# Kernel optimization log

Measured on AMD Instinct MI355X. Metric: run time of the kernel, lower is better.

Reference implementation:

```python
import jax, jax.numpy as jnp
import numpy as np

N, E, DIN, DOUT = 50000, 625000, 128, 128


def setup_inputs() -> dict:
    key = jax.random.key(0)
    k = jax.random.split(key, 4)
    x = jax.random.normal(k[0], (N, DIN), dtype=jnp.float32)
    edge_index = jax.random.randint(k[1], (2, E), 0, N, dtype=jnp.int32)
    s = 1.0 / np.sqrt(DIN)  # Glorot-ish init like torch Linear
    W_fwd = jax.random.uniform(k[2], (DIN, DOUT), jnp.float32, -s, s)
    W_bwd = jax.random.uniform(k[3], (DIN, DOUT), jnp.float32, -s, s)
    b_fwd = jnp.zeros((DOUT,), jnp.float32)
    b_bwd = jnp.zeros((DOUT,), jnp.float32)
    return {"x": x, "edge_index": edge_index, "W_fwd": W_fwd, "b_fwd": b_fwd,
            "W_bwd": W_bwd, "b_bwd": b_bwd}


def gcn_conv(x, W, b, src, dst, n):
    """PyG GCNConv: add self-loops, symmetric degree norm, gather-scatter aggregate."""
    loops = jnp.arange(n, dtype=src.dtype)
    src2 = jnp.concatenate([src, loops])  # [E+N]
    dst2 = jnp.concatenate([dst, loops])
    ones = jnp.ones(src2.shape[0], dtype=x.dtype)
    deg = jax.ops.segment_sum(ones, dst2, num_segments=n)  # in-degree incl. self-loop
    dinv = jnp.where(deg > 0, jax.lax.rsqrt(deg), 0.0)
    norm = dinv[src2] * dinv[dst2]  # [E+N]
    h = x @ W  # [N, DOUT] dense GEMM before message passing
    msgs = h[src2] * norm[:, None]  # gather + scale, [E+N, DOUT]
    out = jax.ops.segment_sum(msgs, dst2, num_segments=n)  # scatter-add
    return out + b


def reference(x, edge_index, W_fwd, b_fwd, W_bwd, b_bwd):
    src, dst = edge_index[0], edge_index[1]
    n = x.shape[0]
    x_forward = gcn_conv(x, W_fwd, b_fwd, src, dst, n)
    # reversed edge direction for the backward diffusion conv
    x_backward = gcn_conv(x, W_bwd, b_bwd, dst, src, n)
    # dropout omitted (eval mode / deterministic reference)
    return jax.nn.relu(x_forward + x_backward)
```

## Files before the change

### kernel.cpp

```cpp
#include <hip/hip_runtime.h>
#include <hip/hip_bf16.h>
#include <cstdint>

static constexpr int BLK      = 256;
static constexpr int CAP      = 40;
static constexpr int BINSHIFT = 8;
static constexpr int BINNODES = 1 << BINSHIFT;
static constexpr int BINCAP   = BINNODES * CAP / 2;
static constexpr int EPB      = 2048;
static constexpr int OVMAX    = 1024;
static constexpr int NB2MAX   = 512;

typedef __attribute__((ext_vector_type(8))) short bf16x8;
typedef __attribute__((ext_vector_type(4))) float f32x4;

__device__ __forceinline__ float bf16lo(uint32_t u) { return __uint_as_float(u << 16); }
__device__ __forceinline__ float bf16hi(uint32_t u) { return __uint_as_float(u & 0xffff0000u); }
__device__ __forceinline__ unsigned short f2bf(float f) {
    __hip_bfloat16 h = __float2bfloat16(f);
    return *(unsigned short*)&h;
}

__global__ __launch_bounds__(BLK) void k_bin(
        const int* __restrict__ src, const int* __restrict__ dst, int ne,
        uint32_t* __restrict__ pair, int* __restrict__ gcnt,
        int* __restrict__ ovcnt, int* __restrict__ ovlist, int nbins) {
    __shared__ uint32_t stage[EPB * 2];
    __shared__ int hist[NB2MAX];
    __shared__ int lofs[NB2MAX];
    __shared__ int gbase[NB2MAX];
    __shared__ int chunk[NB2MAX / 8];
    const int tid = threadIdx.x, bid = blockIdx.x;
    const int nb2 = 2 * nbins;
    for (int i = tid; i < nb2; i += BLK) hist[i] = 0;
    __syncthreads();

    int s[8], d[8];
    const int e0 = bid * EPB + tid;
#pragma unroll
    for (int k = 0; k < 8; ++k) {
        int e = e0 + k * BLK;
        bool v = e < ne;
        s[k] = v ? src[e] : -1;
        d[k] = v ? dst[e] : -1;
        if (v) {
            atomicAdd(&hist[d[k] >> BINSHIFT], 1);
            atomicAdd(&hist[nbins + (s[k] >> BINSHIFT)], 1);
        }
    }
    __syncthreads();

    const int nch = (nb2 + 7) >> 3;
    if (tid < nch) {
        int a = 0, base = tid << 3;
#pragma unroll
        for (int k = 0; k < 8; ++k) { int idx = base + k; if (idx < nb2) a += hist[idx]; }
        chunk[tid] = a;
    }
    __syncthreads();
    if (tid == 0) { int a = 0; for (int c = 0; c < nch; ++c) { int t = chunk[c]; chunk[c] = a; a += t; } }
    __syncthreads();
    for (int i = tid; i < nb2; i += BLK) {
        int a = chunk[i >> 3];
        for (int k = (i >> 3) << 3; k < i; ++k) a += hist[k];
        lofs[i] = a;
    }
    __syncthreads();
    for (int i = tid; i < nb2; i += BLK) {
        int c = hist[i];
        gbase[i] = c ? atomicAdd(&gcnt[i], c) : 0;
        hist[i] = lofs[i];
    }
    __syncthreads();
#pragma unroll
    for (int k = 0; k < 8; ++k) {
        if (s[k] >= 0) {
            int b0 = d[k] >> BINSHIFT;
            int p0 = atomicAdd(&hist[b0], 1);
            stage[p0] = ((uint32_t)d[k] << 16) | (uint32_t)s[k];
            int b1 = nbins + (s[k] >> BINSHIFT);
            int p1 = atomicAdd(&hist[b1], 1);
            stage[p1] = ((uint32_t)s[k] << 16) | (uint32_t)d[k];
        }
    }
    __syncthreads();
    int nval = ne - bid * EPB; if (nval > EPB) nval = EPB; if (nval < 0) nval = 0;
    const int total = 2 * nval;
    for (int i = tid; i < total; i += BLK) {
        int lo = 0, hi = nb2 - 1;
        while (lo < hi) { int mid = (lo + hi + 1) >> 1; if (lofs[mid] <= i) lo = mid; else hi = mid - 1; }
        int gidx = gbase[lo] + (i - lofs[lo]);
        if (gidx < BINCAP)
            pair[(size_t)lo * BINCAP + gidx] = stage[i];
        else {
            int node = (int)(stage[i] >> 16);
            int q = atomicAdd(ovcnt, 1);
            if (q < OVMAX) ovlist[q] = (node << 1) | (lo >= nbins ? 1 : 0);
        }
    }
}

__global__ __launch_bounds__(BLK) void k_build_conv(
        uint32_t* __restrict__ pair, const int* __restrict__ gcnt,
        int* __restrict__ cnt_f, int* __restrict__ cnt_b,
        float* __restrict__ dinv_f, float* __restrict__ dinv_b,
        int* __restrict__ ovcnt, int* __restrict__ ovlist,
        const float* __restrict__ x, uint32_t* __restrict__ xb32, int nxw, int gxc,
        const float* __restrict__ Wf, const float* __restrict__ Wb,
        unsigned short* __restrict__ WTf, unsigned short* __restrict__ WTb,
        int n, int nbins) {
    const int bid = blockIdx.x, tid = threadIdx.x;
    const int nb2 = 2 * nbins;
    if (bid < nb2) {
        __shared__ unsigned short buck[BINNODES * CAP];
        __shared__ int lcnt[BINNODES];
        lcnt[tid] = 0;
        __syncthreads();
        int count = gcnt[bid]; if (count > BINCAP) count = BINCAP;
        const uint32_t* pb = pair + (size_t)bid * BINCAP;
        const int dir = bid >= nbins ? 1 : 0;
        for (int i = tid; i < count; i += BLK) {
            uint32_t p = pb[i];
            int l = (p >> 16) & (BINNODES - 1);
            int r = atomicAdd(&lcnt[l], 1);
            if (r < CAP) buck[l * CAP + r] = (unsigned short)(p & 0xffffu);
            else {
                int q = atomicAdd(ovcnt, 1);
                if (q < OVMAX)
                    ovlist[q] = (((((bid - dir * nbins) << BINSHIFT) + l)) << 1) | dir;
            }
        }
        __syncthreads();
        const int node = ((bid - dir * nbins) << BINSHIFT) + tid;
        if (node < n) {
            int c = lcnt[tid];
            if (dir) { cnt_b[node] = c; dinv_b[node] = rsqrtf(1.0f + (float)c); }
            else     { cnt_f[node] = c; dinv_f[node] = rsqrtf(1.0f + (float)c); }
        }
        uint32_t* seg = pair + (size_t)bid * BINCAP;
        const uint32_t* b32 = (const uint32_t*)buck;
        for (int i = tid; i < BINCAP; i += BLK) seg[i] = b32[i];
        return;
    }
    if (bid < nb2 + gxc) {
        int base = (bid - nb2) * 2048;
        int end = base + 2048; if (end > nxw) end = nxw;
        for (int i = base + tid; i < end; i += BLK) {
            float2 v = ((const float2*)x)[i];
            xb32[i] = ((uint32_t)f2bf(v.y) << 16) | (uint32_t)f2bf(v.x);
        }
        return;
    }
    int wb = bid - nb2 - gxc;
    for (int idx = wb * 2048 + tid; idx < (wb + 1) * 2048; idx += BLK) {
        int c = idx >> 7, k = idx & 127;
        WTf[c * 128 + k] = f2bf(Wf[k * 128 + c]);
        WTb[c * 128 + k] = f2bf(Wb[k * 128 + c]);
    }
}

__device__ __forceinline__ void accum_range(
        int j0, int j1, int ofs, float sc,
        const uint32_t* __restrict__ xb, int lane, float& a0, float& a1) {
    int j = j0;
    for (; j + 8 <= j1; j += 8) {
        int   o0 = __shfl(ofs, j + 0), o1 = __shfl(ofs, j + 1);
        int   o2 = __shfl(ofs, j + 2), o3 = __shfl(ofs, j + 3);
        int   o4 = __shfl(ofs, j + 4), o5 = __shfl(ofs, j + 5);
        int   o6 = __shfl(ofs, j + 6), o7 = __shfl(ofs, j + 7);
        float s0 = __shfl(sc, j + 0), s1 = __shfl(sc, j + 1);
        float s2 = __shfl(sc, j + 2), s3 = __shfl(sc, j + 3);
        float s4 = __shfl(sc, j + 4), s5 = __shfl(sc, j + 5);
        float s6 = __shfl(sc, j + 6), s7 = __shfl(sc, j + 7);
        uint32_t u0 = xb[(size_t)(o0 + lane)], u1 = xb[(size_t)(o1 + lane)];
        uint32_t u2 = xb[(size_t)(o2 + lane)], u3 = xb[(size_t)(o3 + lane)];
        uint32_t u4 = xb[(size_t)(o4 + lane)], u5 = xb[(size_t)(o5 + lane)];
        uint32_t u6 = xb[(size_t)(o6 + lane)], u7 = xb[(size_t)(o7 + lane)];
        a0 = fmaf(s0, bf16lo(u0), a0); a1 = fmaf(s0, bf16hi(u0), a1);
        a0 = fmaf(s1, bf16lo(u1), a0); a1 = fmaf(s1, bf16hi(u1), a1);
        a0 = fmaf(s2, bf16lo(u2), a0); a1 = fmaf(s2, bf16hi(u2), a1);
        a0 = fmaf(s3, bf16lo(u3), a0); a1 = fmaf(s3, bf16hi(u3), a1);
        a0 = fmaf(s4, bf16lo(u4), a0); a1 = fmaf(s4, bf16hi(u4), a1);
        a0 = fmaf(s5, bf16lo(u5), a0); a1 = fmaf(s5, bf16hi(u5), a1);
        a0 = fmaf(s6, bf16lo(u6), a0); a1 = fmaf(s6, bf16hi(u6), a1);
        a0 = fmaf(s7, bf16lo(u7), a0); a1 = fmaf(s7, bf16hi(u7), a1);
    }
    for (; j + 4 <= j1; j += 4) {
        int   o0 = __shfl(ofs, j + 0), o1 = __shfl(ofs, j + 1);
        int   o2 = __shfl(ofs, j + 2), o3 = __shfl(ofs, j + 3);
        float s0 = __shfl(sc, j + 0), s1 = __shfl(sc, j + 1);
        float s2 = __shfl(sc, j + 2), s3 = __shfl(sc, j + 3);
        uint32_t u0 = xb[(size_t)(o0 + lane)], u1 = xb[(size_t)(o1 + lane)];
        uint32_t u2 = xb[(size_t)(o2 + lane)], u3 = xb[(size_t)(o3 + lane)];
        a0 = fmaf(s0, bf16lo(u0), a0); a1 = fmaf(s0, bf16hi(u0), a1);
        a0 = fmaf(s1, bf16lo(u1), a0); a1 = fmaf(s1, bf16hi(u1), a1);
        a0 = fmaf(s2, bf16lo(u2), a0); a1 = fmaf(s2, bf16hi(u2), a1);
        a0 = fmaf(s3, bf16lo(u3), a0); a1 = fmaf(s3, bf16hi(u3), a1);
    }
    for (; j < j1; ++j) {
        int oj = __shfl(ofs, j); float sj = __shfl(sc, j);
        uint32_t uj = xb[(size_t)(oj + lane)];
        a0 = fmaf(sj, bf16lo(uj), a0); a1 = fmaf(sj, bf16hi(uj), a1);
    }
}

__global__ __launch_bounds__(BLK) void k_gather_agg(
        const int* __restrict__ cnt_f, const int* __restrict__ cnt_b,
        const unsigned short* __restrict__ adj_f,
        const unsigned short* __restrict__ adj_b,
        const float* __restrict__ dinv_f, const float* __restrict__ dinv_b,
        const uint32_t* __restrict__ xb32,
        uint32_t* __restrict__ agg32,
        int n, int gnode,
        const int* __restrict__ ovcnt, const int* __restrict__ ovlist,
        const int* __restrict__ src, const int* __restrict__ dst, int ne) {
    const int bid = blockIdx.x;
    if (bid < gnode) {
        const int wave = threadIdx.x >> 6;
        const int lane = threadIdx.x & 63;
        const int node = bid * 4 + wave;
        if (node >= n) return;

        int cf = cnt_f[node], cb = cnt_b[node];
        if (cf > CAP || cb > CAP) return;

        float dvsf = dinv_f[node], dvsb = dinv_b[node];
        uint32_t uv = xb32[(size_t)node * 64 + lane];
        float accf0 = dvsf * dvsf * bf16lo(uv), accf1 = dvsf * dvsf * bf16hi(uv);
        float accb0 = dvsb * dvsb * bf16lo(uv), accb1 = dvsb * dvsb * bf16hi(uv);

        const int mt = cf + cb;
        if (mt <= 64) {
            int ofs = 0; float sc = 0.f;
            if (lane < cf) {
                int nb = adj_f[node * CAP + lane];
                ofs = nb * 64;
                sc  = dvsf * dinv_f[nb];
            } else if (lane < mt) {
                int nb = adj_b[node * CAP + (lane - cf)];
                ofs = nb * 64;
                sc  = dvsb * dinv_b[nb];
            }
            accum_range(0,  cf, ofs, sc, xb32, lane, accf0, accf1);
            accum_range(cf, mt, ofs, sc, xb32, lane, accb0, accb1);
        } else {
            for (int j = 0; j < cf; ++j) {
                int nb = adj_f[node * CAP + j];
                float dj = dvsf * dinv_f[nb];
                uint32_t u = xb32[(size_t)nb * 64 + lane];
                accf0 = fmaf(dj, bf16lo(u), accf0); accf1 = fmaf(dj, bf16hi(u), accf1);
            }
            for (int j = 0; j < cb; ++j) {
                int nb = adj_b[node * CAP + j];
                float dj = dvsb * dinv_b[nb];
                uint32_t u = xb32[(size_t)nb * 64 + lane];
                accb0 = fmaf(dj, bf16lo(u), accb0); accb1 = fmaf(dj, bf16hi(u), accb1);
            }
        }
        agg32[(size_t)node * 128 + lane] =
            ((uint32_t)f2bf(accf1) << 16) | (uint32_t)f2bf(accf0);
        agg32[(size_t)node * 128 + 64 + lane] =
            ((uint32_t)f2bf(accb1) << 16) | (uint32_t)f2bf(accb0);
        return;
    }

    int nov = *ovcnt; if (nov > OVMAX) nov = OVMAX;
    if (nov == 0) return;
    __shared__ int lst[4096];
    __shared__ int lc;
    const int tid = threadIdx.x;
    for (int i = bid - gnode; i < nov; i += 8) {
        int node = ovlist[i] >> 1;
        for (int d2 = 0; d2 < 2; ++d2) {
            const int* key = d2 ? src : dst;
            const int* val = d2 ? dst : src;
            const float* dinv = d2 ? dinv_b : dinv_f;
            float dvs = dinv[node];
            float s0 = 0.f, s1 = 0.f;
            if (tid < 64) {
                uint32_t u = xb32[(size_t)node * 64 + tid];
                s0 = dvs * bf16lo(u); s1 = dvs * bf16hi(u);
            }
            for (int start = 0; start < ne; start += 4096) {
                if (tid == 0) lc = 0;
                __syncthreads();
                int end = min(start + 4096, ne);
                for (int e2 = start + tid; e2 < end; e2 += BLK)
                    if (key[e2] == node) { int q = atomicAdd(&lc, 1); lst[q] = val[e2]; }
                __syncthreads();
                int mm = lc;
                if (tid < 64) {
                    for (int j = 0; j < mm; ++j) {
                        int nb = lst[j];
                        float dv = dinv[nb];
                        uint32_t u = xb32[(size_t)nb * 64 + tid];
                        s0 = fmaf(dv, bf16lo(u), s0);
                        s1 = fmaf(dv, bf16hi(u), s1);
                    }
                }
                __syncthreads();
            }
            if (tid < 64) {
                float a0 = dvs * s0, a1 = dvs * s1;
                agg32[(size_t)node * 128 + d2 * 64 + tid] =
                    ((uint32_t)f2bf(a1) << 16) | (uint32_t)f2bf(a0);
            }
            __syncthreads();
        }
    }
}

__global__ __launch_bounds__(BLK) void k_gemm_out(
        const unsigned short* __restrict__ agg,
        const unsigned short* __restrict__ WTf,
        const unsigned short* __restrict__ WTb,
        const float* __restrict__ bfv, const float* __restrict__ bbv,
        float* __restrict__ out, int n) {
    const int wave = threadIdx.x >> 6, lane = threadIdx.x & 63;
    const int wm = wave >> 1, wh = wave & 1;
    const int q = lane >> 4, t16 = lane & 15;
    const int m0 = blockIdx.x * 32 + wm * 16;
    int arow = m0 + t16; if (arow >= n) arow = n - 1;
    const unsigned short* ra = agg + (size_t)arow * 256;
    bf16x8 af[4], ab[4];
#pragma unroll
    for (int s = 0; s < 4; ++s) {
        af[s] = *(const bf16x8*)(ra + s * 32 + q * 8);
        ab[s] = *(const bf16x8*)(ra + 128 + s * 32 + q * 8);
    }
    __syncthreads();
#pragma unroll
    for (int t = 0; t < 4; ++t) {
        const int col = wh * 64 + t * 16 + t16;
        const unsigned short* wrf = WTf + (size_t)col * 128;
        const unsigned short* wrb = WTb + (size_t)col * 128;
        f32x4 c = {0.f, 0.f, 0.f, 0.f};
#pragma unroll
        for (int s = 0; s < 4; ++s)
            c = __builtin_amdgcn_mfma_f32_16x16x32_bf16(
                    af[s], *(const bf16x8*)(wrf + s * 32 + q * 8), c, 0, 0, 0);
#pragma unroll
        for (int s = 0; s < 4; ++s)
            c = __builtin_amdgcn_mfma_f32_16x16x32_bf16(
                    ab[s], *(const bf16x8*)(wrb + s * 32 + q * 8), c, 0, 0, 0);
        const float bias = bfv[col] + bbv[col];
#pragma unroll
        for (int r = 0; r < 4; ++r) {
            int row = m0 + q * 4 + r;
            if (row < n)
                out[(size_t)row * 128 + col] = fmaxf(c[r] + bias, 0.f);
        }
    }
}

extern "C" void kernel_launch(void* const* d_in, const int* in_sizes, int n_in,
                              void* d_out, int out_size, void* d_ws, size_t ws_size,
                              hipStream_t stream) {
    const float* x  = (const float*)d_in[0];
    const int*   ei = (const int*)d_in[1];
    const float* Wf = (const float*)d_in[2];
    const float* bf = (const float*)d_in[3];
    const float* Wb = (const float*)d_in[4];
    const float* bb = (const float*)d_in[5];

    const int n  = in_sizes[0] / 128;
    const int ne = in_sizes[1] / 2;
    const int* src = ei;
    const int* dst = ei + ne;
    float* out = (float*)d_out;

    const int nbins = (n + BINNODES - 1) >> BINSHIFT;
    const int nb2   = 2 * nbins;

    char* w = (char*)d_ws;
    uint32_t* pair = (uint32_t*)w;              w += (size_t)nb2 * BINCAP * 4;
    uint32_t* xb32 = (uint32_t*)w;              w += (size_t)n * 64 * 4;
    float* dinv_f = (float*)w;                  w += (size_t)n * 4;
    float* dinv_b = (float*)w;                  w += (size_t)n * 4;
    unsigned short* WTf = (unsigned short*)w;   w += 128 * 128 * 2;
    unsigned short* WTb = (unsigned short*)w;   w += 128 * 128 * 2;
    int* cnt_f = (int*)w;                       w += (size_t)n * 4;
    int* cnt_b = (int*)w;                       w += (size_t)n * 4;
    int* gcnt = (int*)w;                        w += (size_t)nb2 * 4;
    int* ovcnt = (int*)w;                       w += 8 * 4;
    int* ovlist = (int*)w;                      w += OVMAX * 4;

    const unsigned short* adj_f = (const unsigned short*)pair;
    const unsigned short* adj_b = adj_f + (size_t)nbins * BINNODES * CAP;
    uint32_t* agg32 = (uint32_t*)d_out;

    const int gbin  = (ne + EPB - 1) / EPB;
    const int gxc   = (n * 64 + 2047) / 2048;
    const int gnode = (n + 3) / 4;
    const int ggo   = (n + 31) / 32;

    hipMemsetAsync(gcnt, 0, (size_t)(nb2 + 8) * 4, stream);

    k_bin<<<gbin, BLK, 0, stream>>>(src, dst, ne, pair, gcnt, ovcnt, ovlist, nbins);

    k_build_conv<<<nb2 + gxc + 8, BLK, 0, stream>>>(pair, gcnt,
                                                    cnt_f, cnt_b, dinv_f, dinv_b,
                                                    ovcnt, ovlist,
                                                    x, xb32, n * 64, gxc,
                                                    Wf, Wb, WTf, WTb, n, nbins);

    k_gather_agg<<<gnode + 8, BLK, 0, stream>>>(cnt_f, cnt_b, adj_f, adj_b,
                                                dinv_f, dinv_b, xb32,
                                                agg32, n, gnode,
                                                ovcnt, ovlist, src, dst, ne);

    k_gemm_out<<<ggo, BLK, 0, stream>>>((const unsigned short*)agg32,
                                        WTf, WTb, bf, bb, out, n);
}
```

Baseline: 199.4 us.

## Fuse x/W conversion into binning kernel and pack per-node metadata

Moves the bf16 conversion of x and the W transposes from the build kernel into the binning kernel, so that independent work overlaps with edge binning and the build kernel only handles the bins. In binning, a per-item bin index is kept in shared memory in place of a binary search over the offsets. Per-node count and dinv for both directions are packed into one 16-byte meta record read with a single load, and the gather step preloads neighbor indices and dinv before the degree check, with forward and backward edges fixed to wave halves of 32 lanes. The trade is more shared memory in the binning kernel, a zero-fill of the bucket array, and a fast path now limited to 32 edges per direction.

```diff
diff --git a/kernel.cpp b/kernel.cpp
--- a/kernel.cpp
+++ b/kernel.cpp
@@ -16,134 +16,99 @@
 
 __device__ __forceinline__ float bf16lo(uint32_t u) { return __uint_as_float(u << 16); }
 __device__ __forceinline__ float bf16hi(uint32_t u) { return __uint_as_float(u & 0xffff0000u); }
+__device__ __forceinline__ float bf16f(unsigned short u) { return __uint_as_float((uint32_t)u << 16); }
 __device__ __forceinline__ unsigned short f2bf(float f) {
     __hip_bfloat16 h = __float2bfloat16(f);
     return *(unsigned short*)&h;
 }
 
-__global__ __launch_bounds__(BLK) void k_bin(
+__global__ __launch_bounds__(BLK) void k_bin_conv(
         const int* __restrict__ src, const int* __restrict__ dst, int ne,
         uint32_t* __restrict__ pair, int* __restrict__ gcnt,
-        int* __restrict__ ovcnt, int* __restrict__ ovlist, int nbins) {
-    __shared__ uint32_t stage[EPB * 2];
-    __shared__ int hist[NB2MAX];
-    __shared__ int lofs[NB2MAX];
-    __shared__ int gbase[NB2MAX];
-    __shared__ int chunk[NB2MAX / 8];
-    const int tid = threadIdx.x, bid = blockIdx.x;
-    const int nb2 = 2 * nbins;
-    for (int i = tid; i < nb2; i += BLK) hist[i] = 0;
-    __syncthreads();
-
-    int s[8], d[8];
-    const int e0 = bid * EPB + tid;
-#pragma unroll
-    for (int k = 0; k < 8; ++k) {
-        int e = e0 + k * BLK;
-        bool v = e < ne;
-        s[k] = v ? src[e] : -1;
-        d[k] = v ? dst[e] : -1;
-        if (v) {
-            atomicAdd(&hist[d[k] >> BINSHIFT], 1);
-            atomicAdd(&hist[nbins + (s[k] >> BINSHIFT)], 1);
-        }
-    }
-    __syncthreads();
-
-    const int nch = (nb2 + 7) >> 3;
-    if (tid < nch) {
-        int a = 0, base = tid << 3;
-#pragma unroll
-        for (int k = 0; k < 8; ++k) { int idx = base + k; if (idx < nb2) a += hist[idx]; }
-        chunk[tid] = a;
-    }
-    __syncthreads();
-    if (tid == 0) { int a = 0; for (int c = 0; c < nch; ++c) { int t = chunk[c]; chunk[c] = a; a += t; } }
-    __syncthreads();
-    for (int i = tid; i < nb2; i += BLK) {
-        int a = chunk[i >> 3];
-        for (int k = (i >> 3) << 3; k < i; ++k) a += hist[k];
-        lofs[i] = a;
-    }
-    __syncthreads();
-    for (int i = tid; i < nb2; i += BLK) {
-        int c = hist[i];
-        gbase[i] = c ? atomicAdd(&gcnt[i], c) : 0;
-        hist[i] = lofs[i];
-    }
-    __syncthreads();
-#pragma unroll
-    for (int k = 0; k < 8; ++k) {
-        if (s[k] >= 0) {
-            int b0 = d[k] >> BINSHIFT;
-            int p0 = atomicAdd(&hist[b0], 1);
-            stage[p0] = ((uint32_t)d[k] << 16) | (uint32_t)s[k];
-            int b1 = nbins + (s[k] >> BINSHIFT);
-            int p1 = atomicAdd(&hist[b1], 1);
-            stage[p1] = ((uint32_t)s[k] << 16) | (uint32_t)d[k];
-        }
-    }
-    __syncthreads();
-    int nval = ne - bid * EPB; if (nval > EPB) nval = EPB; if (nval < 0) nval = 0;
-    const int total = 2 * nval;
-    for (int i = tid; i < total; i += BLK) {
-        int lo = 0, hi = nb2 - 1;
-        while (lo < hi) { int mid = (lo + hi + 1) >> 1; if (lofs[mid] <= i) lo = mid; else hi = mid - 1; }
-        int gidx = gbase[lo] + (i - lofs[lo]);
-        if (gidx < BINCAP)
-            pair[(size_t)lo * BINCAP + gidx] = stage[i];
-        else {
-            int node = (int)(stage[i] >> 16);
-            int q = atomicAdd(ovcnt, 1);
-            if (q < OVMAX) ovlist[q] = (node << 1) | (lo >= nbins ? 1 : 0);
-        }
-    }
-}
-
-__global__ __launch_bounds__(BLK) void k_build_conv(
-        uint32_t* __restrict__ pair, const int* __restrict__ gcnt,
-        int* __restrict__ cnt_f, int* __restrict__ cnt_b,
-        float* __restrict__ dinv_f, float* __restrict__ dinv_b,
-        int* __restrict__ ovcnt, int* __restrict__ ovlist,
+        int* __restrict__ ovcnt, int* __restrict__ ovlist, int nbins, int gbin,
         const float* __restrict__ x, uint32_t* __restrict__ xb32, int nxw, int gxc,
         const float* __restrict__ Wf, const float* __restrict__ Wb,
-        unsigned short* __restrict__ WTf, unsigned short* __restrict__ WTb,
-        int n, int nbins) {
+        unsigned short* __restrict__ WTf, unsigned short* __restrict__ WTb) {
     const int bid = blockIdx.x, tid = threadIdx.x;
-    const int nb2 = 2 * nbins;
-    if (bid < nb2) {
-        __shared__ unsigned short buck[BINNODES * CAP];
-        __shared__ int lcnt[BINNODES];
-        lcnt[tid] = 0;
-        __syncthreads();
-        int count = gcnt[bid]; if (count > BINCAP) count = BINCAP;
-        const uint32_t* pb = pair + (size_t)bid * BINCAP;
-        const int dir = bid >= nbins ? 1 : 0;
-        for (int i = tid; i < count; i += BLK) {
-            uint32_t p = pb[i];
-            int l = (p >> 16) & (BINNODES - 1);
-            int r = atomicAdd(&lcnt[l], 1);
-            if (r < CAP) buck[l * CAP + r] = (unsigned short)(p & 0xffffu);
+    if (bid < gbin) {
+        __shared__ uint32_t stage[EPB * 2];
+        __shared__ unsigned short binof[EPB * 2];
+        __shared__ int hist[NB2MAX];
+        __shared__ int lofs[NB2MAX];
+        __shared__ int gbase[NB2MAX];
+        __shared__ int chunk[NB2MAX / 8];
+        const int nb2 = 2 * nbins;
+        for (int i = tid; i < nb2; i += BLK) hist[i] = 0;
+        __syncthreads();
+
+        int s[8], d[8];
+        const int e0 = bid * EPB + tid;
+#pragma unroll
+        for (int k = 0; k < 8; ++k) {
+            int e = e0 + k * BLK;
+            bool v = e < ne;
+            s[k] = v ? src[e] : -1;
+            d[k] = v ? dst[e] : -1;
+            if (v) {
+                atomicAdd(&hist[d[k] >> BINSHIFT], 1);
+                atomicAdd(&hist[nbins + (s[k] >> BINSHIFT)], 1);
+            }
+        }
+        __syncthreads();
+
+        const int nch = (nb2 + 7) >> 3;
+        if (tid < nch) {
+            int a = 0, base = tid << 3;
+#pragma unroll
+            for (int k = 0; k < 8; ++k) { int idx = base + k; if (idx < nb2) a += hist[idx]; }
+            chunk[tid] = a;
+        }
+        __syncthreads();
+        if (tid == 0) { int a = 0; for (int c = 0; c < nch; ++c) { int t = chunk[c]; chunk[c] = a; a += t; } }
+        __syncthreads();
+        for (int i = tid; i < nb2; i += BLK) {
+            int a = chunk[i >> 3];
+            for (int k = (i >> 3) << 3; k < i; ++k) a += hist[k];
+            lofs[i] = a;
+        }
+        __syncthreads();
+        for (int i = tid; i < nb2; i += BLK) {
+            int c = hist[i];
+            gbase[i] = c ? atomicAdd(&gcnt[i], c) : 0;
+            hist[i] = lofs[i];
+        }
+        __syncthreads();
+#pragma unroll
+        for (int k = 0; k < 8; ++k) {
+            if (s[k] >= 0) {
+                int b0 = d[k] >> BINSHIFT;
+                int p0 = atomicAdd(&hist[b0], 1);
+                stage[p0] = ((uint32_t)d[k] << 16) | (uint32_t)s[k];
+                binof[p0] = (unsigned short)b0;
+                int b1 = nbins + (s[k] >> BINSHIFT);
+                int p1 = atomicAdd(&hist[b1], 1);
+                stage[p1] = ((uint32_t)s[k] << 16) | (uint32_t)d[k];
+                binof[p1] = (unsigned short)b1;
+            }
+        }
+        __syncthreads();
+        int nval = ne - bid * EPB; if (nval > EPB) nval = EPB; if (nval < 0) nval = 0;
+        const int total = 2 * nval;
+        for (int i = tid; i < total; i += BLK) {
+            int b = binof[i];
+            int gidx = gbase[b] + (i - lofs[b]);
+            if (gidx < BINCAP)
+                pair[(size_t)b * BINCAP + gidx] = stage[i];
             else {
+                int node = (int)(stage[i] >> 16);
                 int q = atomicAdd(ovcnt, 1);
-                if (q < OVMAX)
-                    ovlist[q] = (((((bid - dir * nbins) << BINSHIFT) + l)) << 1) | dir;
-            }
-        }
-        __syncthreads();
-        const int node = ((bid - dir * nbins) << BINSHIFT) + tid;
-        if (node < n) {
-            int c = lcnt[tid];
-            if (dir) { cnt_b[node] = c; dinv_b[node] = rsqrtf(1.0f + (float)c); }
-            else     { cnt_f[node] = c; dinv_f[node] = rsqrtf(1.0f + (float)c); }
-        }
-        uint32_t* seg = pair + (size_t)bid * BINCAP;
-        const uint32_t* b32 = (const uint32_t*)buck;
-        for (int i = tid; i < BINCAP; i += BLK) seg[i] = b32[i];
+                if (q < OVMAX) ovlist[q] = (node << 1) | (b >= nbins ? 1 : 0);
+            }
+        }
         return;
     }
-    if (bid < nb2 + gxc) {
-        int base = (bid - nb2) * 2048;
+    if (bid < gbin + gxc) {
+        int base = (bid - gbin) * 2048;
         int end = base + 2048; if (end > nxw) end = nxw;
         for (int i = base + tid; i < end; i += BLK) {
             float2 v = ((const float2*)x)[i];
@@ -151,12 +116,56 @@
         }
         return;
     }
-    int wb = bid - nb2 - gxc;
+    int wb = bid - gbin - gxc;
     for (int idx = wb * 2048 + tid; idx < (wb + 1) * 2048; idx += BLK) {
         int c = idx >> 7, k = idx & 127;
         WTf[c * 128 + k] = f2bf(Wf[k * 128 + c]);
         WTb[c * 128 + k] = f2bf(Wb[k * 128 + c]);
     }
+}
+
+__global__ __launch_bounds__(BLK) void k_build(
+        uint32_t* __restrict__ pair, const int* __restrict__ gcnt,
+        float* __restrict__ dinv_f, float* __restrict__ dinv_b,
+        uint4* __restrict__ meta,
+        int* __restrict__ ovcnt, int* __restrict__ ovlist,
+        int n, int nbins) {
+    const int bid = blockIdx.x, tid = threadIdx.x;
+    __shared__ unsigned short buck[BINNODES * CAP];
+    __shared__ int lcnt[BINNODES];
+    lcnt[tid] = 0;
+    for (int i = tid; i < BINNODES * CAP / 2; i += BLK) ((uint32_t*)buck)[i] = 0;
+    __syncthreads();
+    int count = gcnt[bid]; if (count > BINCAP) count = BINCAP;
+    const uint32_t* pb = pair + (size_t)bid * BINCAP;
+    const int dir = bid >= nbins ? 1 : 0;
+    for (int i = tid; i < count; i += BLK) {
+        uint32_t p = pb[i];
+        int l = (p >> 16) & (BINNODES - 1);
+        int r = atomicAdd(&lcnt[l], 1);
+        if (r < CAP) buck[l * CAP + r] = (unsigned short)(p & 0xffffu);
+        else {
+            int q = atomicAdd(ovcnt, 1);
+            if (q < OVMAX)
+                ovlist[q] = (((((bid - dir * nbins) << BINSHIFT) + l)) << 1) | dir;
+        }
+    }
+    __syncthreads();
+    const int node = ((bid - dir * nbins) << BINSHIFT) + tid;
+    if (node < n) {
+        int c = lcnt[tid];
+        float dv = rsqrtf(1.0f + (float)c);
+        if (dir) {
+            dinv_b[node] = dv;
+            ((uint2*)&meta[node])[1] = make_uint2(__float_as_uint(dv), (uint32_t)c);
+        } else {
+            dinv_f[node] = dv;
+            ((uint2*)&meta[node])[0] = make_uint2(__float_as_uint(dv), (uint32_t)c);
+        }
+    }
+    uint32_t* seg = pair + (size_t)bid * BINCAP;
+    const uint32_t* b32 = (const uint32_t*)buck;
+    for (int i = tid; i < BINCAP; i += BLK) seg[i] = b32[i];
 }
 
 __device__ __forceinline__ void accum_range(
@@ -205,7 +214,7 @@
 }
 
 __global__ __launch_bounds__(BLK) void k_gather_agg(
-        const int* __restrict__ cnt_f, const int* __restrict__ cnt_b,
+        const uint4* __restrict__ meta,
         const unsigned short* __restrict__ adj_f,
         const unsigned short* __restrict__ adj_b,
         const float* __restrict__ dinv_f, const float* __restrict__ dinv_b,
@@ -221,39 +230,38 @@
         const int node = bid * 4 + wave;
         if (node >= n) return;
 
-        int cf = cnt_f[node], cb = cnt_b[node];
+        uint4 mv = meta[node];
+        const int h = lane >> 5, slot = lane & 31;
+        int nb = h ? adj_b[node * CAP + slot] : adj_f[node * CAP + slot];
+        uint32_t uv = xb32[(size_t)node * 64 + lane];
+        float dnb = h ? dinv_b[nb] : dinv_f[nb];
+
+        float dvsf = __uint_as_float(mv.x), dvsb = __uint_as_float(mv.z);
+        int cf = (int)mv.y, cb = (int)mv.w;
         if (cf > CAP || cb > CAP) return;
 
-        float dvsf = dinv_f[node], dvsb = dinv_b[node];
-        uint32_t uv = xb32[(size_t)node * 64 + lane];
-        float accf0 = dvsf * dvsf * bf16lo(uv), accf1 = dvsf * dvsf * bf16hi(uv);
-        float accb0 = dvsb * dvsb * bf16lo(uv), accb1 = dvsb * dvsb * bf16hi(uv);
-
-        const int mt = cf + cb;
-        if (mt <= 64) {
-            int ofs = 0; float sc = 0.f;
-            if (lane < cf) {
-                int nb = adj_f[node * CAP + lane];
-                ofs = nb * 64;
-                sc  = dvsf * dinv_f[nb];
-            } else if (lane < mt) {
-                int nb = adj_b[node * CAP + (lane - cf)];
-                ofs = nb * 64;
-                sc  = dvsb * dinv_b[nb];
-            }
-            accum_range(0,  cf, ofs, sc, xb32, lane, accf0, accf1);
-            accum_range(cf, mt, ofs, sc, xb32, lane, accb0, accb1);
+        float wf = dvsf * dvsf, wb = dvsb * dvsb;
+        float accf0 = wf * bf16lo(uv), accf1 = wf * bf16hi(uv);
+        float accb0 = wb * bf16lo(uv), accb1 = wb * bf16hi(uv);
+
+        if (cf <= 32 && cb <= 32) {
+            float dvs_h = h ? dvsb : dvsf;
+            int   c_h   = h ? cb : cf;
+            float sc  = (slot < c_h) ? dvs_h * dnb : 0.f;
+            int   ofs = nb * 64;
+            accum_range(0,  cf,      ofs, sc, xb32, lane, accf0, accf1);
+            accum_range(32, 32 + cb, ofs, sc, xb32, lane, accb0, accb1);
         } else {
             for (int j = 0; j < cf; ++j) {
-                int nb = adj_f[node * CAP + j];
-                float dj = dvsf * dinv_f[nb];
-                uint32_t u = xb32[(size_t)nb * 64 + lane];
+                int nb2 = adj_f[node * CAP + j];
+                float dj = dvsf * dinv_f[nb2];
+                uint32_t u = xb32[(size_t)nb2 * 64 + lane];
                 accf0 = fmaf(dj, bf16lo(u), accf0); accf1 = fmaf(dj, bf16hi(u), accf1);
             }
             for (int j = 0; j < cb; ++j) {
-                int nb = adj_b[node * CAP + j];
-                float dj = dvsb * dinv_b[nb];
-                uint32_t u = xb32[(size_t)nb * 64 + lane];
+                int nb2 = adj_b[node * CAP + j];
+                float dj = dvsb * dinv_b[nb2];
+                uint32_t u = xb32[(size_t)nb2 * 64 + lane];
                 accb0 = fmaf(dj, bf16lo(u), accb0); accb1 = fmaf(dj, bf16hi(u), accb1);
             }
         }
@@ -266,7 +274,7 @@
 
     int nov = *ovcnt; if (nov > OVMAX) nov = OVMAX;
     if (nov == 0) return;
-    __shared__ int lst[4096];
+    __shared__ int lst[2048];
     __shared__ int lc;
     const int tid = threadIdx.x;
     for (int i = bid - gnode; i < nov; i += 8) {
@@ -281,10 +289,10 @@
                 uint32_t u = xb32[(size_t)node * 64 + tid];
                 s0 = dvs * bf16lo(u); s1 = dvs * bf16hi(u);
             }
-            for (int start = 0; start < ne; start += 4096) {
+            for (int start = 0; start < ne; start += 2048) {
                 if (tid == 0) lc = 0;
                 __syncthreads();
-                int end = min(start + 4096, ne);
+                int end = min(start + 2048, ne);
                 for (int e2 = start + tid; e2 < end; e2 += BLK)
                     if (key[e2] == node) { int q = atomicAdd(&lc, 1); lst[q] = val[e2]; }
                 __syncthreads();
@@ -375,12 +383,11 @@
     char* w = (char*)d_ws;
     uint32_t* pair = (uint32_t*)w;              w += (size_t)nb2 * BINCAP * 4;
     uint32_t* xb32 = (uint32_t*)w;              w += (size_t)n * 64 * 4;
+    uint4* meta = (uint4*)w;                    w += (size_t)n * 16;
     float* dinv_f = (float*)w;                  w += (size_t)n * 4;
     float* dinv_b = (float*)w;                  w += (size_t)n * 4;
     unsigned short* WTf = (unsigned short*)w;   w += 128 * 128 * 2;
     unsigned short* WTb = (unsigned short*)w;   w += 128 * 128 * 2;
-    int* cnt_f = (int*)w;                       w += (size_t)n * 4;
-    int* cnt_b = (int*)w;                       w += (size_t)n * 4;
     int* gcnt = (int*)w;                        w += (size_t)nb2 * 4;
     int* ovcnt = (int*)w;                       w += 8 * 4;
     int* ovlist = (int*)w;                      w += OVMAX * 4;
@@ -396,15 +403,16 @@
 
     hipMemsetAsync(gcnt, 0, (size_t)(nb2 + 8) * 4, stream);
 
-    k_bin<<<gbin, BLK, 0, stream>>>(src, dst, ne, pair, gcnt, ovcnt, ovlist, nbins);
-
-    k_build_conv<<<nb2 + gxc + 8, BLK, 0, stream>>>(pair, gcnt,
-                                                    cnt_f, cnt_b, dinv_f, dinv_b,
-                                                    ovcnt, ovlist,
-                                                    x, xb32, n * 64, gxc,
-                                                    Wf, Wb, WTf, WTb, n, nbins);
-
-    k_gather_agg<<<gnode + 8, BLK, 0, stream>>>(cnt_f, cnt_b, adj_f, adj_b,
+    k_bin_conv<<<gbin + gxc + 8, BLK, 0, stream>>>(src, dst, ne,
+                                                   pair, gcnt, ovcnt, ovlist,
+                                                   nbins, gbin,
+                                                   x, xb32, n * 64, gxc,
+                                                   Wf, Wb, WTf, WTb);
+
+    k_build<<<nb2, BLK, 0, stream>>>(pair, gcnt, dinv_f, dinv_b, meta,
+                                     ovcnt, ovlist, n, nbins);
+
+    k_gather_agg<<<gnode + 8, BLK, 0, stream>>>(meta, adj_f, adj_b,
                                                 dinv_f, dinv_b, xb32,
                                                 agg32, n, gnode,
                                                 ovcnt, ovlist, src, dst, ne);
```

New measurement: 187.3 us. 6.1% less time.
